# Kernel optimization log

Measured on AMD Instinct MI355X. Metric: run time of the kernel, lower is better.

The kernel has to match this reference:

```python
import jax, jax.numpy as jnp
import numpy as np

N = 50000      # nodes
E = 1_600_000  # edges
DIN, HID, OUT, H = 128, 32, 32, 4


def _glorot(key, shape):
    fan_in, fan_out = shape[0], shape[1] if len(shape) > 1 else shape[0]
    s = jnp.sqrt(6.0 / (fan_in + fan_out)).astype(jnp.float32)
    return jax.random.uniform(key, shape, jnp.float32, -s, s)


def setup_inputs() -> dict:
    key = jax.random.key(0)
    ks = jax.random.split(key, 16)
    inp = {
        "x": jax.random.normal(ks[0], (N, DIN), jnp.float32),
        "edge_index": jax.random.randint(ks[1], (2, E), 0, N, dtype=jnp.int32),
        "edge_weight": jax.random.uniform(ks[2], (E, 1), jnp.float32),
        # layer 1: in=DIN, heads=H, out=HID, concat=True
        "Wl1": _glorot(ks[3], (DIN, H * HID)),
        "Wr1": _glorot(ks[4], (DIN, H * HID)),
        "We1": _glorot(ks[5], (1, H * HID)),
        "att1": _glorot(ks[6], (H, HID)),
        "b1": jnp.zeros((H * HID,), jnp.float32),
        # layer 2: in=H*HID, heads=H, out=OUT, concat=False (mean over heads)
        "Wl2": _glorot(ks[7], (H * HID, H * OUT)),
        "Wr2": _glorot(ks[8], (H * HID, H * OUT)),
        "We2": _glorot(ks[9], (1, H * OUT)),
        "att2": _glorot(ks[10], (H, OUT)),
        "b2": jnp.zeros((OUT,), jnp.float32),
    }
    return inp


def gatv2_layer(x, edge_index, edge_weight, Wl, Wr, We, att, b, concat):
    """Faithful PyG GATv2Conv (share_weights=False, negative_slope=0.2,
    add_self_loops=True with fill_value='mean' for edge_attr)."""
    n = x.shape[0]
    heads, c = att.shape
    src, dst = edge_index[0], edge_index[1]
    # add self loops with mean edge weight (PyG default when edge_dim is set)
    loop = jnp.arange(n, dtype=edge_index.dtype)
    src = jnp.concatenate([src, loop])
    dst = jnp.concatenate([dst, loop])
    ew = jnp.concatenate(
        [edge_weight, jnp.full((n, edge_weight.shape[1]), jnp.mean(edge_weight), edge_weight.dtype)], axis=0)

    xl = (x @ Wl).reshape(n, heads, c)   # source transform (lin_l)
    xr = (x @ Wr).reshape(n, heads, c)   # target transform (lin_r)
    e_feat = (ew @ We).reshape(-1, heads, c)

    z = jax.nn.leaky_relu(xl[src] + xr[dst] + e_feat, 0.2)   # [E', H, C]
    logits = jnp.einsum('ehc,hc->eh', z, att)                # [E', H]

    # segment softmax over incoming edges of each target node
    m = jax.ops.segment_max(logits, dst, num_segments=n)
    m = jnp.where(jnp.isfinite(m), m, 0.0)
    p = jnp.exp(logits - m[dst])
    denom = jax.ops.segment_sum(p, dst, num_segments=n)
    alpha = p / (denom[dst] + 1e-16)                          # [E', H]

    out = jax.ops.segment_sum(xl[src] * alpha[..., None], dst, num_segments=n)  # [N, H, C]
    out = out.reshape(n, heads * c) if concat else out.mean(axis=1)
    return out + b


def reference(x, edge_index, edge_weight, Wl1, Wr1, We1, att1, b1,
              Wl2, Wr2, We2, att2, b2):
    h = gatv2_layer(x, edge_index, edge_weight, Wl1, Wr1, We1, att1, b1, concat=True)
    h = jax.nn.elu(h)
    out = gatv2_layer(h, edge_index, edge_weight, Wl2, Wr2, We2, att2, b2, concat=False)
    return out
```

## Files before the change

### kernel.cpp

```cpp
#include <hip/hip_runtime.h>
#include <hip/hip_fp16.h>
#include <math.h>
#include <type_traits>


typedef _Float16 half8 __attribute__((ext_vector_type(8)));
typedef float floatx4 __attribute__((ext_vector_type(4)));

__global__ __launch_bounds__(256) void bucket_hist_sum(
    const int* __restrict__ dst, const float* __restrict__ ew,
    int* __restrict__ bcnt, float* __restrict__ sumbuf, int E) {
    __shared__ int h[256];
    h[threadIdx.x] = 0;
    __syncthreads();
    float s = 0.f;
    for (int i = blockIdx.x * blockDim.x + threadIdx.x; i < E; i += gridDim.x * blockDim.x) {
        atomicAdd(&h[dst[i] >> 8], 1);
        s += ew[i];
    }
#pragma unroll
    for (int off = 1; off <= 32; off <<= 1)
        s += __shfl_xor(s, off, 64);
    if ((threadIdx.x & 63) == 0)
        atomicAdd(sumbuf, s);
    __syncthreads();
    int v = h[threadIdx.x];
    if (v) atomicAdd(&bcnt[threadIdx.x], v);
}

__global__ __launch_bounds__(1024) void partition_kernel(
    const int* __restrict__ src, const int* __restrict__ dst, const float* __restrict__ ew,
    const int* __restrict__ bcnt, int* __restrict__ bcur, int* __restrict__ bbase,
    int2* __restrict__ srec, int E, int NBK) {
    __shared__ int ex[256];
    __shared__ int h[256];
    __shared__ int gb[256];
    const int t = threadIdx.x;

    if (t < 256) ex[t] = (t < NBK) ? bcnt[t] : 0;
    __syncthreads();
    for (int off = 1; off < 256; off <<= 1) {
        int y = 0;
        if (t < 256 && t >= off) y = ex[t - off];
        __syncthreads();
        if (t < 256) ex[t] += y;
        __syncthreads();
    }
    if (blockIdx.x == 0 && t <= NBK)
        bbase[t] = (t < 256) ? (ex[t] - ((t < NBK) ? bcnt[t] : 0))
                             : ex[255];
    if (t < 256) h[t] = 0;
    __syncthreads();

    const int base = blockIdx.x * 8192;
    int d[8], sv[8];
    float wv[8];
#pragma unroll
    for (int j = 0; j < 8; j++) {
        int i = base + t + j * 1024;
        if (i < E) {
            d[j] = dst[i];
            sv[j] = src[i];
            wv[j] = ew[i];
            atomicAdd(&h[d[j] >> 8], 1);
        } else {
            d[j] = -1;
        }
    }
    __syncthreads();
    if (t < 256) {
        int cntt = h[t];
        int exb = ex[t] - ((t < NBK) ? bcnt[t] : 0);
        if (cntt) gb[t] = exb + atomicAdd(&bcur[t], cntt);
        h[t] = 0;
    }
    __syncthreads();
#pragma unroll
    for (int j = 0; j < 8; j++) {
        if (d[j] >= 0) {
            int b = d[j] >> 8;
            int r = atomicAdd(&h[b], 1);
            int pos = gb[b] + r;
            srec[pos] = make_int2(sv[j] | ((d[j] & 255) << 20), __float_as_int(wv[j]));
        }
    }
}

__global__ __launch_bounds__(1024) void build_csr_kernel(
    const int2* __restrict__ srec, const int* __restrict__ bbase,
    const float* __restrict__ sumbuf, int* __restrict__ rowp,
    int2* __restrict__ crec, int N, int E) {
    __shared__ int h4[4][256];
    __shared__ int sc[256];
    __shared__ int cur[256];
    const int t = threadIdx.x;
    const int grp = t >> 8, sub = t & 255;
    h4[grp][sub] = 0;
    __syncthreads();
    const int b = blockIdx.x;
    const int e0 = bbase[b], e1 = bbase[b + 1];
    for (int i = e0 + t; i < e1; i += 1024)
        atomicAdd(&h4[grp][(srec[i].x >> 20) & 255], 1);
    __syncthreads();
    int deg = 0;
    if (t < 256) {
        deg = h4[0][t] + h4[1][t] + h4[2][t] + h4[3][t];
        int node = (b << 8) + t;
        sc[t] = (node < N) ? (deg + 1) : 0;
    }
    __syncthreads();
    for (int off = 1; off < 256; off <<= 1) {
        int y = 0;
        if (t < 256 && t >= off) y = sc[t - off];
        __syncthreads();
        if (t < 256) sc[t] += y;
        __syncthreads();
    }
    const int base = bbase[b] + (b << 8);
    if (t < 256) {
        int node = (b << 8) + t;
        if (node < N) {
            int rp = base + sc[t] - (deg + 1);
            rowp[node] = rp;
            cur[t] = rp;
            crec[rp + deg] = make_int2(node, __float_as_int(sumbuf[0] * (1.0f / (float)E)));
            if (node == N - 1) rowp[N] = E + N;
        }
    }
    __syncthreads();
    for (int i = e0 + t; i < e1; i += 1024) {
        int2 rec = srec[i];
        int dlow = (rec.x >> 20) & 255;
        int pos = atomicAdd(&cur[dlow], 1);
        crec[pos] = make_int2(rec.x & 0xFFFFF, rec.y);
    }
}

__global__ __launch_bounds__(256) void prep_w2_kernel(
    const float* __restrict__ Wa1, const float* __restrict__ Wb1,
    const float* __restrict__ Wa2, const float* __restrict__ Wb2,
    _Float16* __restrict__ Wh1, _Float16* __restrict__ Wh2,
    int* __restrict__ bcnt, int* __restrict__ bcur) {
    const int bid = blockIdx.x;
    if (bid == 0 && threadIdx.x < 260) bcnt[threadIdx.x] = 0;
    if (bid == 1 && threadIdx.x < 260) bcur[threadIdx.x] = 0;
    const int sel = bid >> 7;
    const float* Wa = sel ? Wa2 : Wa1;
    const float* Wb = sel ? Wb2 : Wb1;
    _Float16* Wh = sel ? Wh2 : Wh1;
    int tid = (bid & 127) * 256 + threadIdx.x;
    int j = tid & 7;
    int lane = (tid >> 3) & 63;
    int f = tid >> 9;
    int kk = f & 3;
    int ct = f >> 2;
    int col = ct * 16 + (lane & 15);
    int k = kk * 32 + ((lane >> 4) << 3) + j;
    float v = (col < 128) ? Wa[k * 128 + col] : Wb[k * 128 + (col - 128)];
    Wh[tid] = (_Float16)v;
}

template <typename T>
__global__ __launch_bounds__(256) void gemm_mfma_kernel(
    const T* __restrict__ X, const _Float16* __restrict__ Wh,
    __half* __restrict__ Yh, float* __restrict__ Yb, int N) {
    __shared__ _Float16 Xs[64 * 128];
    const int tid = threadIdx.x;
    const int lane = tid & 63;
    const int w = tid >> 6;
    const int rb = blockIdx.x * 64;

    half8 wf[4][4];
#pragma unroll
    for (int ct = 0; ct < 4; ct++)
#pragma unroll
        for (int kk = 0; kk < 4; kk++)
            wf[ct][kk] = *(const half8*)(Wh + (size_t)(((w * 4 + ct) * 4 + kk) * 512 + lane * 8));

    if constexpr (std::is_same<T, float>::value) {
#pragma unroll
        for (int it = 0; it < 8; it++) {
            int c = it * 256 + tid;
            int row = c >> 5;
            int f4 = c & 31;
            float4 v = make_float4(0.f, 0.f, 0.f, 0.f);
            if (rb + row < N)
                v = ((const float4*)X)[(size_t)(rb + row) * 32 + f4];
            _Float16 h[4] = {(_Float16)v.x, (_Float16)v.y, (_Float16)v.z, (_Float16)v.w};
            int byteoff = row * 256 + ((f4 * 8) ^ ((row & 7) << 4));
            *(uint2*)((char*)Xs + byteoff) = *(uint2*)h;
        }
    } else {
#pragma unroll
        for (int it = 0; it < 4; it++) {
            int c = it * 256 + tid;
            int row = c >> 4;
            int f16 = c & 15;
            int4 v = make_int4(0, 0, 0, 0);
            if (rb + row < N)
                v = ((const int4*)X)[(size_t)(rb + row) * 16 + f16];
            int byteoff = row * 256 + ((f16 * 16) ^ ((row & 7) << 4));
            *(int4*)((char*)Xs + byteoff) = v;
        }
    }
    __syncthreads();

    floatx4 acc[4][4];
#pragma unroll
    for (int ct = 0; ct < 4; ct++)
#pragma unroll
        for (int rt = 0; rt < 4; rt++)
            acc[ct][rt] = (floatx4){0.f, 0.f, 0.f, 0.f};

#pragma unroll
    for (int kk = 0; kk < 4; kk++) {
        half8 xf[4];
#pragma unroll
        for (int rt = 0; rt < 4; rt++) {
            int row = rt * 16 + (lane & 15);
            int kb = kk * 64 + ((lane >> 4) << 4);
            int off = row * 256 + (kb ^ ((row & 7) << 4));
            xf[rt] = *(const half8*)((const char*)Xs + off);
        }
#pragma unroll
        for (int ct = 0; ct < 4; ct++)
#pragma unroll
            for (int rt = 0; rt < 4; rt++)
                acc[ct][rt] = __builtin_amdgcn_mfma_f32_16x16x32_f16(
                    wf[ct][kk], xf[rt], acc[ct][rt], 0, 0, 0);
    }

    const int rsub = lane & 15;
    const int c4 = (lane >> 4) << 2;
#pragma unroll
    for (int ct = 0; ct < 4; ct++) {
        int gct = w * 4 + ct;
#pragma unroll
        for (int rt = 0; rt < 4; rt++) {
            int row = rb + rt * 16 + rsub;
            if (row < N) {
                floatx4 a = acc[ct][rt];
                if (gct < 8) {
                    int col = gct * 16 + c4;
                    __half2 hp[2];
                    hp[0] = __floats2half2_rn(a[0], a[1]);
                    hp[1] = __floats2half2_rn(a[2], a[3]);
                    *(uint2*)(Yh + (size_t)row * 128 + col) = *(uint2*)hp;
                } else {
                    int col = (gct - 8) * 16 + c4;
                    *(float4*)(Yb + (size_t)row * 128 + col) =
                        make_float4(a[0], a[1], a[2], a[3]);
                }
            }
        }
    }
}

template <int CTRL>
__device__ __forceinline__ float dpp_sum_step(float v) {
    int t = __builtin_amdgcn_update_dpp(0, __float_as_int(v), CTRL, 0xF, 0xF, true);
    return v + __int_as_float(t);
}

__device__ __forceinline__ float2 cvt_h2(unsigned u) {
    __half2 h = *(__half2*)&u;
    return __half22float2(h);
}

__global__ __launch_bounds__(256) void agg_kernel(
    const __half* __restrict__ xlh, const float* __restrict__ xr,
    const int* __restrict__ rowp, const int2* __restrict__ crec,
    const float* __restrict__ We, const float* __restrict__ att, const float* __restrict__ bias,
    void* __restrict__ out, int N, int mode) {
    const int wid = threadIdx.x >> 6;
    const int lane = threadIdx.x & 63;
    const int n = blockIdx.x * 4 + wid;
    if (n >= N) return;
    const int g = lane >> 4;
    const int q = lane & 15;
    const int c0 = q << 3;
    const float LOG2E = 1.4426950408889634f;

    float we[8], xv[8], at6[8], at4[8];
    {
        float4 wA = *(const float4*)(We + c0);
        float4 wB = *(const float4*)(We + c0 + 4);
        we[0]=wA.x; we[1]=wA.y; we[2]=wA.z; we[3]=wA.w;
        we[4]=wB.x; we[5]=wB.y; we[6]=wB.z; we[7]=wB.w;
        float4 rA = *(const float4*)(xr + (size_t)n * 128 + c0);
        float4 rB = *(const float4*)(xr + (size_t)n * 128 + c0 + 4);
        xv[0]=rA.x; xv[1]=rA.y; xv[2]=rA.z; xv[3]=rA.w;
        xv[4]=rB.x; xv[5]=rB.y; xv[6]=rB.z; xv[7]=rB.w;
        float4 aA = *(const float4*)(att + c0);
        float4 aB = *(const float4*)(att + c0 + 4);
        float av[8] = {aA.x, aA.y, aA.z, aA.w, aB.x, aB.y, aB.z, aB.w};
#pragma unroll
        for (int c = 0; c < 8; c++) {
            at6[c] = 0.6f * LOG2E * av[c];
            at4[c] = 0.4f * LOG2E * av[c];
        }
    }

    float acc[8];
#pragma unroll
    for (int c = 0; c < 8; c++) acc[c] = 0.f;
    float l0 = 0.f;

    const int e0 = __builtin_amdgcn_readfirstlane(rowp[n]);
    const int e1 = __builtin_amdgcn_readfirstlane(rowp[n + 1]);
    const int cnt = e1 - e0;
    const int T = (cnt + 3) >> 2;

    auto recload = [&](int i) -> int2 {
        int idx = e0 + (i << 2) + g;
        idx = (idx < e1 - 1) ? idx : (e1 - 1);
        return crec[idx];
    };
    auto gatherx = [&](int s) -> int4 {
        return *(const int4*)(xlh + (size_t)s * 128 + c0);
    };
    auto process = [&](int4 xh, float w, bool valid) {
        float2 x01 = cvt_h2(xh.x), x23 = cvt_h2(xh.y);
        float2 x45 = cvt_h2(xh.z), x67 = cvt_h2(xh.w);
        float xs[8] = {x01.x, x01.y, x23.x, x23.y, x45.x, x45.y, x67.x, x67.y};
        float p = 0.f;
#pragma unroll
        for (int c = 0; c < 8; c++) {
            float z = xs[c] + fmaf(w, we[c], xv[c]);
            p = fmaf(at6[c], z, fmaf(at4[c], fabsf(z), p));
        }
        p = dpp_sum_step<0xB1>(p);
        p = dpp_sum_step<0x4E>(p);
        float qe = valid ? __builtin_amdgcn_exp2f(p) : 0.f;
        l0 += qe;
#pragma unroll
        for (int c = 0; c < 8; c++) acc[c] = fmaf(qe, xs[c], acc[c]);
    };

    int2 r0 = recload(0), r1 = recload(1), r2 = recload(2), r3 = recload(3);
    int4 x0 = gatherx(r0.x), x1 = gatherx(r1.x);
    for (int i = 0; i < T; ++i) {
        int2 r4 = recload(i + 4);
        int4 x2 = gatherx(r2.x);
        process(x0, __int_as_float(r0.y), (e0 + (i << 2) + g) < e1);
        r0 = r1; r1 = r2; r2 = r3; r3 = r4;
        x0 = x1; x1 = x2;
    }

    l0 += __shfl_xor(l0, 16, 64);
    l0 += __shfl_xor(l0, 32, 64);
#pragma unroll
    for (int c = 0; c < 8; c++) {
        acc[c] += __shfl_xor(acc[c], 16, 64);
        acc[c] += __shfl_xor(acc[c], 32, 64);
    }
    float rdenom = 1.0f / (l0 + 1e-16f);
    float r[8];
#pragma unroll
    for (int c = 0; c < 8; c++) r[c] = acc[c] * rdenom;

    if (mode == 0) {
        if (g == 0) {
            float4 bA = *(const float4*)(bias + c0);
            float4 bB = *(const float4*)(bias + c0 + 4);
            float bv[8] = {bA.x, bA.y, bA.z, bA.w, bB.x, bB.y, bB.z, bB.w};
            float o[8];
#pragma unroll
            for (int c = 0; c < 8; c++) {
                float v = r[c] + bv[c];
                o[c] = (v > 0.f) ? v : (__expf(v) - 1.f);
            }
            __half2 p0 = __floats2half2_rn(o[0], o[1]);
            __half2 p1 = __floats2half2_rn(o[2], o[3]);
            __half2 p2 = __floats2half2_rn(o[4], o[5]);
            __half2 p3 = __floats2half2_rn(o[6], o[7]);
            int4 pk = make_int4(*(int*)&p0, *(int*)&p1, *(int*)&p2, *(int*)&p3);
            *(int4*)((__half*)out + (size_t)n * 128 + c0) = pk;
        }
    } else {
#pragma unroll
        for (int c = 0; c < 8; c++) {
            r[c] += __shfl_xor(r[c], 4, 64);
            r[c] += __shfl_xor(r[c], 8, 64);
        }
        if (lane < 4) {
            int w0 = lane << 3;
            float4 bA = *(const float4*)(bias + w0);
            float4 bB = *(const float4*)(bias + w0 + 4);
            float bv[8] = {bA.x, bA.y, bA.z, bA.w, bB.x, bB.y, bB.z, bB.w};
            float o[8];
#pragma unroll
            for (int c = 0; c < 8; c++) o[c] = 0.25f * r[c] + bv[c];
            float* op = (float*)out + (size_t)n * 32 + w0;
            *(float4*)op       = make_float4(o[0], o[1], o[2], o[3]);
            *(float4*)(op + 4) = make_float4(o[4], o[5], o[6], o[7]);
        }
    }
}

extern "C" void kernel_launch(void* const* d_in, const int* in_sizes, int n_in,
                              void* d_out, int out_size, void* d_ws, size_t ws_size,
                              hipStream_t stream) {
    const float* x    = (const float*)d_in[0];
    const int*  eidx  = (const int*)d_in[1];
    const float* ew   = (const float*)d_in[2];
    const float* Wl1  = (const float*)d_in[3];
    const float* Wr1  = (const float*)d_in[4];
    const float* We1  = (const float*)d_in[5];
    const float* att1 = (const float*)d_in[6];
    const float* b1   = (const float*)d_in[7];
    const float* Wl2  = (const float*)d_in[8];
    const float* Wr2  = (const float*)d_in[9];
    const float* We2  = (const float*)d_in[10];
    const float* att2 = (const float*)d_in[11];
    const float* b2   = (const float*)d_in[12];

    const int N = in_sizes[0] / 128;
    const int E = in_sizes[1] / 2;
    const int* src = eidx;
    const int* dst = eidx + E;
    const int NBK = (N + 255) >> 8;

    char* p = (char*)d_ws;
    auto alloc = [&](size_t bytes) -> void* {
        void* r = (void*)p;
        p += (bytes + 255) & ~(size_t)255;
        return r;
    };
    __half* xlh   = (__half*)alloc((size_t)N * 128 * sizeof(__half));
    float* xr     = (float*)alloc((size_t)N * 128 * sizeof(float));
    __half* h1h   = (__half*)alloc((size_t)N * 128 * sizeof(float));
    int2*  crec   = (int2*)alloc((size_t)(E + N + 64) * sizeof(int2));
    int*   rowp   = (int*)alloc((size_t)(N + 1) * sizeof(int));
    int*   bcnt   = (int*)alloc(260 * sizeof(int));
    float* sumbuf = (float*)(bcnt + 256);
    int*   bbase  = (int*)alloc(260 * sizeof(int));
    int*   bcur   = (int*)alloc(260 * sizeof(int));
    _Float16* Wh1 = (_Float16*)alloc(32768 * sizeof(_Float16));
    _Float16* Wh2 = (_Float16*)alloc(32768 * sizeof(_Float16));
    int2*  srec   = (int2*)h1h;

    prep_w2_kernel<<<256, 256, 0, stream>>>(Wl1, Wr1, Wl2, Wr2, Wh1, Wh2,
                                            bcnt, bcur);

    bucket_hist_sum<<<1024, 256, 0, stream>>>(dst, ew, bcnt, sumbuf, E);
    partition_kernel<<<(E + 8191) / 8192, 1024, 0, stream>>>(
        src, dst, ew, bcnt, bcur, bbase, srec, E, NBK);
    build_csr_kernel<<<NBK, 1024, 0, stream>>>(srec, bbase, sumbuf, rowp,
                                               crec, N, E);

    gemm_mfma_kernel<float><<<(N + 63) / 64, 256, 0, stream>>>(x, Wh1, xlh, xr, N);
    agg_kernel<<<(N + 3) / 4, 256, 0, stream>>>(xlh, xr, rowp, crec,
                                                We1, att1, b1, (void*)h1h, N, 0);
    gemm_mfma_kernel<_Float16><<<(N + 63) / 64, 256, 0, stream>>>(
        (const _Float16*)h1h, Wh2, xlh, xr, N);
    agg_kernel<<<(N + 3) / 4, 256, 0, stream>>>(xlh, xr, rowp, crec,
                                                We2, att2, b2, d_out, N, 1);
}
```

Baseline: 344.4 us.

## Make projection GEMM persistent with register prefetch of next row tile

The MFMA projection GEMM now launches half as many blocks, and each block loops over two 64-row tiles. Weight fragments are loaded into registers once per block and reused across tiles. While the current tile computes, the next tile's input rows are prefetched into registers. This amortizes weight loading and overlaps global loads with MFMA work, at the cost of higher register pressure and fewer concurrent blocks.

```diff
diff --git a/kernel.cpp b/kernel.cpp
--- a/kernel.cpp
+++ b/kernel.cpp
@@ -163,12 +163,11 @@
 template <typename T>
 __global__ __launch_bounds__(256) void gemm_mfma_kernel(
     const T* __restrict__ X, const _Float16* __restrict__ Wh,
-    __half* __restrict__ Yh, float* __restrict__ Yb, int N) {
+    __half* __restrict__ Yh, float* __restrict__ Yb, int N, int NT) {
     __shared__ _Float16 Xs[64 * 128];
     const int tid = threadIdx.x;
     const int lane = tid & 63;
     const int w = tid >> 6;
-    const int rb = blockIdx.x * 64;
 
     half8 wf[4][4];
 #pragma unroll
@@ -177,79 +176,110 @@
         for (int kk = 0; kk < 4; kk++)
             wf[ct][kk] = *(const half8*)(Wh + (size_t)(((w * 4 + ct) * 4 + kk) * 512 + lane * 8));
 
-    if constexpr (std::is_same<T, float>::value) {
-#pragma unroll
-        for (int it = 0; it < 8; it++) {
-            int c = it * 256 + tid;
-            int row = c >> 5;
-            int f4 = c & 31;
-            float4 v = make_float4(0.f, 0.f, 0.f, 0.f);
-            if (rb + row < N)
-                v = ((const float4*)X)[(size_t)(rb + row) * 32 + f4];
-            _Float16 h[4] = {(_Float16)v.x, (_Float16)v.y, (_Float16)v.z, (_Float16)v.w};
-            int byteoff = row * 256 + ((f4 * 8) ^ ((row & 7) << 4));
-            *(uint2*)((char*)Xs + byteoff) = *(uint2*)h;
-        }
-    } else {
-#pragma unroll
-        for (int it = 0; it < 4; it++) {
-            int c = it * 256 + tid;
-            int row = c >> 4;
-            int f16 = c & 15;
-            int4 v = make_int4(0, 0, 0, 0);
-            if (rb + row < N)
-                v = ((const int4*)X)[(size_t)(rb + row) * 16 + f16];
-            int byteoff = row * 256 + ((f16 * 16) ^ ((row & 7) << 4));
-            *(int4*)((char*)Xs + byteoff) = v;
-        }
-    }
-    __syncthreads();
-
-    floatx4 acc[4][4];
-#pragma unroll
-    for (int ct = 0; ct < 4; ct++)
-#pragma unroll
-        for (int rt = 0; rt < 4; rt++)
-            acc[ct][rt] = (floatx4){0.f, 0.f, 0.f, 0.f};
-
-#pragma unroll
-    for (int kk = 0; kk < 4; kk++) {
-        half8 xf[4];
-#pragma unroll
-        for (int rt = 0; rt < 4; rt++) {
-            int row = rt * 16 + (lane & 15);
-            int kb = kk * 64 + ((lane >> 4) << 4);
-            int off = row * 256 + (kb ^ ((row & 7) << 4));
-            xf[rt] = *(const half8*)((const char*)Xs + off);
-        }
+    float4 pf[8];
+    int4   pg[4];
+
+    auto prefetch = [&](int tile) {
+        if (tile >= NT) return;
+        const int rb = tile * 64;
+        if constexpr (std::is_same<T, float>::value) {
+#pragma unroll
+            for (int it = 0; it < 8; it++) {
+                int c = it * 256 + tid;
+                int row = c >> 5;
+                int f4 = c & 31;
+                pf[it] = make_float4(0.f, 0.f, 0.f, 0.f);
+                if (rb + row < N)
+                    pf[it] = ((const float4*)X)[(size_t)(rb + row) * 32 + f4];
+            }
+        } else {
+#pragma unroll
+            for (int it = 0; it < 4; it++) {
+                int c = it * 256 + tid;
+                int row = c >> 4;
+                int f16 = c & 15;
+                pg[it] = make_int4(0, 0, 0, 0);
+                if (rb + row < N)
+                    pg[it] = ((const int4*)X)[(size_t)(rb + row) * 16 + f16];
+            }
+        }
+    };
+
+    prefetch(blockIdx.x);
+
+    for (int tile = blockIdx.x; tile < NT; tile += gridDim.x) {
+        const int rb = tile * 64;
+        __syncthreads();
+        if constexpr (std::is_same<T, float>::value) {
+#pragma unroll
+            for (int it = 0; it < 8; it++) {
+                int c = it * 256 + tid;
+                int row = c >> 5;
+                int f4 = c & 31;
+                float4 v = pf[it];
+                _Float16 h[4] = {(_Float16)v.x, (_Float16)v.y, (_Float16)v.z, (_Float16)v.w};
+                int byteoff = row * 256 + ((f4 * 8) ^ ((row & 7) << 4));
+                *(uint2*)((char*)Xs + byteoff) = *(uint2*)h;
+            }
+        } else {
+#pragma unroll
+            for (int it = 0; it < 4; it++) {
+                int c = it * 256 + tid;
+                int row = c >> 4;
+                int f16 = c & 15;
+                int byteoff = row * 256 + ((f16 * 16) ^ ((row & 7) << 4));
+                *(int4*)((char*)Xs + byteoff) = pg[it];
+            }
+        }
+        __syncthreads();
+        prefetch(tile + gridDim.x);
+
+        floatx4 acc[4][4];
 #pragma unroll
         for (int ct = 0; ct < 4; ct++)
 #pragma unroll
             for (int rt = 0; rt < 4; rt++)
-                acc[ct][rt] = __builtin_amdgcn_mfma_f32_16x16x32_f16(
-                    wf[ct][kk], xf[rt], acc[ct][rt], 0, 0, 0);
-    }
-
-    const int rsub = lane & 15;
-    const int c4 = (lane >> 4) << 2;
-#pragma unroll
-    for (int ct = 0; ct < 4; ct++) {
-        int gct = w * 4 + ct;
-#pragma unroll
-        for (int rt = 0; rt < 4; rt++) {
-            int row = rb + rt * 16 + rsub;
-            if (row < N) {
-                floatx4 a = acc[ct][rt];
-                if (gct < 8) {
-                    int col = gct * 16 + c4;
-                    __half2 hp[2];
-                    hp[0] = __floats2half2_rn(a[0], a[1]);
-                    hp[1] = __floats2half2_rn(a[2], a[3]);
-                    *(uint2*)(Yh + (size_t)row * 128 + col) = *(uint2*)hp;
-                } else {
-                    int col = (gct - 8) * 16 + c4;
-                    *(float4*)(Yb + (size_t)row * 128 + col) =
-                        make_float4(a[0], a[1], a[2], a[3]);
+                acc[ct][rt] = (floatx4){0.f, 0.f, 0.f, 0.f};
+
+#pragma unroll
+        for (int kk = 0; kk < 4; kk++) {
+            half8 xf[4];
+#pragma unroll
+            for (int rt = 0; rt < 4; rt++) {
+                int row = rt * 16 + (lane & 15);
+                int kb = kk * 64 + ((lane >> 4) << 4);
+                int off = row * 256 + (kb ^ ((row & 7) << 4));
+                xf[rt] = *(const half8*)((const char*)Xs + off);
+            }
+#pragma unroll
+            for (int ct = 0; ct < 4; ct++)
+#pragma unroll
+                for (int rt = 0; rt < 4; rt++)
+                    acc[ct][rt] = __builtin_amdgcn_mfma_f32_16x16x32_f16(
+                        wf[ct][kk], xf[rt], acc[ct][rt], 0, 0, 0);
+        }
+
+        const int rsub = lane & 15;
+        const int c4 = (lane >> 4) << 2;
+#pragma unroll
+        for (int ct = 0; ct < 4; ct++) {
+            int gct = w * 4 + ct;
+#pragma unroll
+            for (int rt = 0; rt < 4; rt++) {
+                int row = rb + rt * 16 + rsub;
+                if (row < N) {
+                    floatx4 a = acc[ct][rt];
+                    if (gct < 8) {
+                        int col = gct * 16 + c4;
+                        __half2 hp[2];
+                        hp[0] = __floats2half2_rn(a[0], a[1]);
+                        hp[1] = __floats2half2_rn(a[2], a[3]);
+                        *(uint2*)(Yh + (size_t)row * 128 + col) = *(uint2*)hp;
+                    } else {
+                        int col = (gct - 8) * 16 + c4;
+                        *(float4*)(Yb + (size_t)row * 128 + col) =
+                            make_float4(a[0], a[1], a[2], a[3]);
+                    }
                 }
             }
         }
@@ -420,6 +450,8 @@
     const int* src = eidx;
     const int* dst = eidx + E;
     const int NBK = (N + 255) >> 8;
+    const int NT  = (N + 63) / 64;
+    const int GG  = (NT + 1) / 2;
 
     char* p = (char*)d_ws;
     auto alloc = [&](size_t bytes) -> void* {
@@ -449,11 +481,11 @@
     build_csr_kernel<<<NBK, 1024, 0, stream>>>(srec, bbase, sumbuf, rowp,
                                                crec, N, E);
 
-    gemm_mfma_kernel<float><<<(N + 63) / 64, 256, 0, stream>>>(x, Wh1, xlh, xr, N);
+    gemm_mfma_kernel<float><<<GG, 256, 0, stream>>>(x, Wh1, xlh, xr, N, NT);
     agg_kernel<<<(N + 3) / 4, 256, 0, stream>>>(xlh, xr, rowp, crec,
                                                 We1, att1, b1, (void*)h1h, N, 0);
-    gemm_mfma_kernel<_Float16><<<(N + 63) / 64, 256, 0, stream>>>(
-        (const _Float16*)h1h, Wh2, xlh, xr, N);
+    gemm_mfma_kernel<_Float16><<<GG, 256, 0, stream>>>(
+        (const _Float16*)h1h, Wh2, xlh, xr, N, NT);
     agg_kernel<<<(N + 3) / 4, 256, 0, stream>>>(xlh, xr, rowp, crec,
                                                 We2, att2, b2, d_out, N, 1);
 }
```

After: 338.4 us. No clear change (-1.7%).
